# Performance work log

Measured on AMD Instinct MI355X. Metric: run time of the kernel, lower is better.

Reference implementation:

```python
import jax, jax.numpy as jnp
import numpy as np

EPS = 1e-08


def _l2norm(x):
    return x / (jnp.linalg.norm(x, axis=-1, keepdims=True) + EPS)


def _mlp(x, weights):
    # weights: list of (W, b); gelu between layers, none after last
    n = len(weights)
    for i, (W, b) in enumerate(weights):
        x = x @ W + b
        if i < n - 1:
            x = jax.nn.gelu(x)  # approximate gelu, matches jax.nn.gelu default
    return x


def setup_inputs() -> dict:
    key = jax.random.key(0)
    ks = jax.random.split(key, 16)
    N, A, L, K = 65536, 32, 256, 1024
    enc_dims = [A, 512, 1024, L]
    dec_dims = [L, 1024, 512, A]

    def lin(k, din, dout):
        kw, kb = jax.random.split(k)
        W = jax.random.normal(kw, (din, dout), jnp.float32) / np.sqrt(din)
        b = jnp.zeros((dout,), jnp.float32)
        return W, b

    inp = {}
    inp["action"] = jax.random.normal(ks[0], (N, A), jnp.float32)
    inp["dim_weights"] = jax.random.uniform(ks[1], (A,), jnp.float32)
    for i in range(3):
        W, b = lin(ks[2 + i], enc_dims[i], enc_dims[i + 1])
        inp[f"enc_w{i}"], inp[f"enc_b{i}"] = W, b
    for i in range(3):
        W, b = lin(ks[5 + i], dec_dims[i], dec_dims[i + 1])
        inp[f"dec_w{i}"], inp[f"dec_b{i}"] = W, b
    cb = jax.random.normal(ks[8], (K, L), jnp.float32) * 0.1
    inp["codebook"] = _l2norm(cb)
    return inp


def reference(action, dim_weights,
              enc_w0, enc_b0, enc_w1, enc_b1, enc_w2, enc_b2,
              dec_w0, dec_b0, dec_w1, dec_b1, dec_w2, dec_b2,
              codebook):
    enc = [(enc_w0, enc_b0), (enc_w1, enc_b1), (enc_w2, enc_b2)]
    dec = [(dec_w0, dec_b0), (dec_w1, dec_b1), (dec_w2, dec_b2)]

    z_e = _l2norm(_mlp(action, enc))                       # [N, L]
    cb = _l2norm(codebook)                                 # [K, L]
    # squared euclidean distances [N, K]
    dists = (jnp.sum(z_e * z_e, axis=-1, keepdims=True)
             - 2.0 * z_e @ cb.T
             + jnp.sum(cb * cb, axis=-1))
    code_idx = jnp.argmin(dists, axis=-1)                  # [N]
    z_q = cb[code_idx]                                     # [N, L]

    z_q_ste = z_e + jax.lax.stop_gradient(z_q - z_e)
    action_hat = _mlp(z_q_ste, dec)                        # [N, A]

    sq_err = (action - action_hat) ** 2 * dim_weights
    recon_loss = jnp.mean(sq_err)
    codebook_loss = jnp.mean((jax.lax.stop_gradient(z_e) - z_q) ** 2)
    commit_loss = jnp.mean((z_e - jax.lax.stop_gradient(z_q)) ** 2)
    return action_hat, code_idx, recon_loss, codebook_loss, commit_loss
```

## Files before the change

### kernel.cpp

```cpp
#include <hip/hip_runtime.h>
#include <math.h>

#define N_ROWS 65536

typedef short short8 __attribute__((ext_vector_type(8)));
typedef float f32x4 __attribute__((ext_vector_type(4)));

__device__ __forceinline__ float gelu_f(float x) {
  float x3 = x * x * x;
  float t = tanhf(0.7978845608028654f * (x + 0.044715f * x3));
  return 0.5f * x * (1.0f + t);
}

__device__ __forceinline__ unsigned short f2bf(float f) {
  unsigned u = __float_as_uint(f);
  unsigned r = u + 0x7fffu + ((u >> 16) & 1u);
  return (unsigned short)(r >> 16);
}
__device__ __forceinline__ float bf2f(unsigned short h) {
  return __uint_as_float(((unsigned)h) << 16);
}

__device__ __forceinline__ void split3(float v, unsigned short& p0,
                                       unsigned short& p1, unsigned short& p2) {
  p0 = f2bf(v);
  float r = v - bf2f(p0);
  p1 = f2bf(r);
  r -= bf2f(p1);
  p2 = f2bf(r);
}

__device__ __forceinline__ void split3f(float v, unsigned short& p0,
                                        unsigned short& p1, unsigned short& p2) {
  unsigned u = __float_as_uint(v);
  unsigned h0 = (u + 0x8000u) & 0xffff0000u;
  float r = v - __uint_as_float(h0);
  unsigned u1 = __float_as_uint(r);
  unsigned h1 = (u1 + 0x8000u) & 0xffff0000u;
  float r2 = r - __uint_as_float(h1);
  p0 = (unsigned short)(h0 >> 16);
  p1 = (unsigned short)(h1 >> 16);
  p2 = f2bf(r2);
}

__device__ __forceinline__ void split2f(float v, unsigned short& p0,
                                        unsigned short& p1) {
  unsigned u = __float_as_uint(v);
  unsigned h0 = (u + 0x8000u) & 0xffff0000u;
  float r = v - __uint_as_float(h0);
  p0 = (unsigned short)(h0 >> 16);
  p1 = f2bf(r);
}

__device__ __forceinline__ f32x4 mfma16(short8 a, short8 b, f32x4 c) {
  return __builtin_amdgcn_mfma_f32_16x16x32_bf16(a, b, c, 0, 0, 0);
}

template <bool GELU>
__global__ __launch_bounds__(256) void gemm_kernel(
    const float* __restrict__ A, const float* __restrict__ W,
    const float* __restrict__ bias, float* __restrict__ C,
    int din, int dout) {
  __shared__ float As[16][132];
  __shared__ float Ws[16][132];
  int t = threadIdx.x;
  int tx = t & 15, ty = t >> 4;
  int c0 = blockIdx.x * 128;
  int r0 = blockIdx.y * 128;

  float acc[8][8];
#pragma unroll
  for (int i = 0; i < 8; ++i)
#pragma unroll
    for (int j = 0; j < 8; ++j) acc[i][j] = 0.0f;

  int kchunks = din >> 4;
  for (int kc = 0; kc < kchunks; ++kc) {
    int k0 = kc << 4;
    __syncthreads();
#pragma unroll
    for (int it = 0; it < 2; ++it) {
      int id = t + it * 256;
      int r = id >> 2;
      int kq = (id & 3) * 4;
      float4 v = *(const float4*)&A[(long)(r0 + r) * din + (k0 + kq)];
      As[kq + 0][r] = v.x; As[kq + 1][r] = v.y;
      As[kq + 2][r] = v.z; As[kq + 3][r] = v.w;
      int k = id >> 5;
      int cq = (id & 31) * 4;
      float4 w = *(const float4*)&W[(long)(k0 + k) * dout + (c0 + cq)];
      *(float4*)&Ws[k][cq] = w;
    }
    __syncthreads();
#pragma unroll
    for (int k = 0; k < 16; ++k) {
      float av[8], bv[8];
      *(float4*)&av[0] = *(const float4*)&As[k][ty * 4];
      *(float4*)&av[4] = *(const float4*)&As[k][ty * 4 + 64];
      *(float4*)&bv[0] = *(const float4*)&Ws[k][tx * 4];
      *(float4*)&bv[4] = *(const float4*)&Ws[k][tx * 4 + 64];
#pragma unroll
      for (int i = 0; i < 8; ++i)
#pragma unroll
        for (int j = 0; j < 8; ++j)
          acc[i][j] = fmaf(av[i], bv[j], acc[i][j]);
    }
  }

  float bbv[8];
  *(float4*)&bbv[0] = *(const float4*)&bias[c0 + tx * 4];
  *(float4*)&bbv[4] = *(const float4*)&bias[c0 + tx * 4 + 64];
#pragma unroll
  for (int i = 0; i < 8; ++i) {
    long row = r0 + ty * 4 + (i & 3) + ((i >> 2) * 64);
    float o[8];
#pragma unroll
    for (int j = 0; j < 8; ++j) {
      float v = acc[i][j] + bbv[j];
      o[j] = GELU ? gelu_f(v) : v;
    }
    *(float4*)&C[row * dout + c0 + tx * 4] = *(float4*)&o[0];
    *(float4*)&C[row * dout + c0 + tx * 4 + 64] = *(float4*)&o[4];
  }
}

__global__ void frag_pack_kernel(const float* __restrict__ W,
                                 unsigned short* __restrict__ Bf,
                                 int K, int N) {
  int l = threadIdx.x;
  int m = l & 15, q = l >> 4;
  int cb = blockIdx.x, kb = blockIdx.y;
  unsigned short s0[8], s1[8], s2[8];
#pragma unroll
  for (int j = 0; j < 8; ++j) {
    float v = W[(long)(kb * 32 + q * 8 + j) * N + cb * 16 + m];
    split3(v, s0[j], s1[j], s2[j]);
  }
  size_t base = ((size_t)cb * (K / 32) + kb) * 3 * 512;
  *(short8*)&Bf[base + 0 * 512 + l * 8] = *(short8*)s0;
  *(short8*)&Bf[base + 1 * 512 + l * 8] = *(short8*)s1;
  *(short8*)&Bf[base + 2 * 512 + l * 8] = *(short8*)s2;
}

__global__ void frag_pack2_t(const float* __restrict__ cbn,
                             unsigned short* __restrict__ Bf) {
  int l = threadIdx.x;
  int m = l & 15, q = l >> 4;
  int cb = blockIdx.x, kb = blockIdx.y;
  unsigned short s0[8], s1[8];
  const float* src = cbn + (long)(cb * 16 + m) * 256 + kb * 32 + q * 8;
#pragma unroll
  for (int j = 0; j < 8; ++j) split2f(src[j], s0[j], s1[j]);
  size_t base = ((size_t)(cb * 8 + kb) * 2) * 512;
  *(short8*)&Bf[base + l * 8] = *(short8*)s0;
  *(short8*)&Bf[base + 512 + l * 8] = *(short8*)s1;
}

template <bool GELU>
__global__ __launch_bounds__(256) void mfma3_gemm(
    const float* __restrict__ A, const unsigned short* __restrict__ Bf,
    const float* __restrict__ bias, float* __restrict__ C,
    int K, int dout) {
  __shared__ unsigned short A_f[3 * 2 * 4 * 512];
  int t = threadIdx.x;
  int lane = t & 63, wave = t >> 6;
  int q = lane >> 4, m = lane & 15;
  int wrb = wave >> 1;
  int wr = wrb * 64, wc = (wave & 1) * 64;
  long r0 = (long)blockIdx.y * 128;
  int c0 = blockIdx.x * 128;
  int kchunks = K >> 5;

  f32x4 acc[4][4];
#pragma unroll
  for (int i = 0; i < 4; ++i)
#pragma unroll
    for (int j = 0; j < 4; ++j) acc[i][j] = (f32x4){0.f, 0.f, 0.f, 0.f};

  int rs = t >> 1, hs = (t & 1) * 16;
  const float* aptr = A + (r0 + rs) * K + hs;
  int cb0 = (c0 + wc) >> 4;
  int xw = (rs >> 4) & 3, wrbw = rs >> 6, mw = rs & 15;
  int g0 = ((t & 1) * 2 + 0) * 16 + mw;
  int g1 = ((t & 1) * 2 + 1) * 16 + mw;
  int wb0 = (0 * 2 + wrbw) * 4 + xw;
  int wb1 = (1 * 2 + wrbw) * 4 + xw;
  int wb2 = (2 * 2 + wrbw) * 4 + xw;

  for (int kb = 0; kb < kchunks; ++kb) {
    __syncthreads();
    {
      int kt = kb << 5;
      float fv[16];
      *(float4*)&fv[0] = *(const float4*)(aptr + kt + 0);
      *(float4*)&fv[4] = *(const float4*)(aptr + kt + 4);
      *(float4*)&fv[8] = *(const float4*)(aptr + kt + 8);
      *(float4*)&fv[12] = *(const float4*)(aptr + kt + 12);
      unsigned short a0[16], a1[16], a2[16];
#pragma unroll
      for (int i = 0; i < 16; ++i) split3f(fv[i], a0[i], a1[i], a2[i]);
      *(uint4*)&A_f[wb0 * 512 + g0 * 8] = ((uint4*)a0)[0];
      *(uint4*)&A_f[wb0 * 512 + g1 * 8] = ((uint4*)a0)[1];
      *(uint4*)&A_f[wb1 * 512 + g0 * 8] = ((uint4*)a1)[0];
      *(uint4*)&A_f[wb1 * 512 + g1 * 8] = ((uint4*)a1)[1];
      *(uint4*)&A_f[wb2 * 512 + g0 * 8] = ((uint4*)a2)[0];
      *(uint4*)&A_f[wb2 * 512 + g1 * 8] = ((uint4*)a2)[1];
    }
    __syncthreads();
    short8 af[3][4];
#pragma unroll
    for (int p = 0; p < 3; ++p)
#pragma unroll
      for (int x = 0; x < 4; ++x)
        af[p][x] = *(const short8*)&A_f[((p * 2 + wrb) * 4 + x) * 512 + lane * 8];
#pragma unroll
    for (int ct = 0; ct < 4; ++ct) {
      size_t fb = ((size_t)(cb0 + ct) * kchunks + kb) * 3 * 512 + lane * 8;
      short8 b0 = *(const short8*)&Bf[fb];
      short8 b1 = *(const short8*)&Bf[fb + 512];
      short8 b2 = *(const short8*)&Bf[fb + 1024];
#pragma unroll
      for (int rt = 0; rt < 4; ++rt) {
        acc[rt][ct] = mfma16(af[0][rt], b0, acc[rt][ct]);
        acc[rt][ct] = mfma16(af[0][rt], b1, acc[rt][ct]);
        acc[rt][ct] = mfma16(af[1][rt], b0, acc[rt][ct]);
        acc[rt][ct] = mfma16(af[0][rt], b2, acc[rt][ct]);
        acc[rt][ct] = mfma16(af[1][rt], b1, acc[rt][ct]);
        acc[rt][ct] = mfma16(af[2][rt], b0, acc[rt][ct]);
      }
    }
  }

#pragma unroll
  for (int ct = 0; ct < 4; ++ct) {
    long col = c0 + wc + ct * 16 + m;
    float bv = bias[col];
#pragma unroll
    for (int rt = 0; rt < 4; ++rt) {
      long rowb = r0 + wr + rt * 16 + q * 4;
#pragma unroll
      for (int r = 0; r < 4; ++r) {
        float v = acc[rt][ct][r] + bv;
        if (GELU) v = gelu_f(v);
        C[(rowb + r) * dout + col] = v;
      }
    }
  }
}

__global__ __launch_bounds__(256) void dist2_mfma(
    const float* __restrict__ z_e, const unsigned short* __restrict__ cbf,
    int* __restrict__ idxc, int* __restrict__ fixcnt, int* __restrict__ fixlist) {
  __shared__ unsigned short A_f[2 * 8 * 4 * 512];
  __shared__ float Lv1[64][4], Lv2[64][4];
  __shared__ int Lc1[64][4];
  int t = threadIdx.x;
  int lane = t & 63, wave = t >> 6;
  int q = lane >> 4, m = lane & 15;
  long r0 = (long)blockIdx.x * 64;

#pragma unroll
  for (int it = 0; it < 4; ++it) {
    int kb = it * 2 + (t >> 7);
    int rs = (t & 127) >> 1, hs = (t & 1) * 16;
    const float* ap = z_e + (r0 + rs) * 256 + kb * 32 + hs;
    float fv[16];
    *(float4*)&fv[0] = *(const float4*)(ap + 0);
    *(float4*)&fv[4] = *(const float4*)(ap + 4);
    *(float4*)&fv[8] = *(const float4*)(ap + 8);
    *(float4*)&fv[12] = *(const float4*)(ap + 12);
    unsigned short a0[16], a1[16];
#pragma unroll
    for (int i = 0; i < 16; ++i) split2f(fv[i], a0[i], a1[i]);
    int x = rs >> 4, mm = rs & 15;
    int ga = ((t & 1) * 2 + 0) * 16 + mm;
    int gb = ((t & 1) * 2 + 1) * 16 + mm;
    int b0 = ((0 * 8 + kb) * 4 + x) * 512;
    int b1 = ((1 * 8 + kb) * 4 + x) * 512;
    *(uint4*)&A_f[b0 + ga * 8] = ((uint4*)a0)[0];
    *(uint4*)&A_f[b0 + gb * 8] = ((uint4*)a0)[1];
    *(uint4*)&A_f[b1 + ga * 8] = ((uint4*)a1)[0];
    *(uint4*)&A_f[b1 + gb * 8] = ((uint4*)a1)[1];
  }
  __syncthreads();

  float v1[4][4], v2[4][4];
  int c1[4][4];
#pragma unroll
  for (int i = 0; i < 4; ++i)
#pragma unroll
    for (int j = 0; j < 4; ++j) { v1[i][j] = -3.4e38f; v2[i][j] = -3.4e38f; c1[i][j] = 0; }

  for (int ctp = 0; ctp < 4; ++ctp) {
    f32x4 acc[4][4];
#pragma unroll
    for (int i = 0; i < 4; ++i)
#pragma unroll
      for (int j = 0; j < 4; ++j) acc[i][j] = (f32x4){0.f, 0.f, 0.f, 0.f};

    for (int kb = 0; kb < 8; ++kb) {
      short8 af0[4], af1[4];
#pragma unroll
      for (int rt = 0; rt < 4; ++rt) {
        af0[rt] = *(const short8*)&A_f[((0 * 8 + kb) * 4 + rt) * 512 + lane * 8];
        af1[rt] = *(const short8*)&A_f[((1 * 8 + kb) * 4 + rt) * 512 + lane * 8];
      }
      short8 bf0[4], bf1[4];
#pragma unroll
      for (int cs = 0; cs < 4; ++cs) {
        int cb = ctp * 16 + (cs >> 1) * 8 + wave * 2 + (cs & 1);
        size_t fb = ((size_t)(cb * 8 + kb) * 2) * 512 + lane * 8;
        bf0[cs] = *(const short8*)&cbf[fb];
        bf1[cs] = *(const short8*)&cbf[fb + 512];
      }
#pragma unroll
      for (int rt = 0; rt < 4; ++rt)
#pragma unroll
        for (int cs = 0; cs < 4; ++cs) {
          acc[rt][cs] = mfma16(af0[rt], bf0[cs], acc[rt][cs]);
          acc[rt][cs] = mfma16(af0[rt], bf1[cs], acc[rt][cs]);
          acc[rt][cs] = mfma16(af1[rt], bf0[cs], acc[rt][cs]);
        }
    }
#pragma unroll
    for (int rt = 0; rt < 4; ++rt)
#pragma unroll
      for (int cs = 0; cs < 4; ++cs) {
        int colb = ctp * 256 + (cs >> 1) * 128 + wave * 32 + (cs & 1) * 16 + m;
#pragma unroll
        for (int r = 0; r < 4; ++r) {
          float v = acc[rt][cs][r];
          float nv2 = fmaxf(v2[rt][r], fminf(v, v1[rt][r]));
          if (v > v1[rt][r]) { c1[rt][r] = colb; v1[rt][r] = v; }
          v2[rt][r] = nv2;
        }
      }
  }

#pragma unroll
  for (int off = 1; off <= 8; off <<= 1) {
#pragma unroll
    for (int rt = 0; rt < 4; ++rt)
#pragma unroll
      for (int r = 0; r < 4; ++r) {
        float ov1 = __shfl_xor(v1[rt][r], off);
        float ov2 = __shfl_xor(v2[rt][r], off);
        int oc1 = __shfl_xor(c1[rt][r], off);
        float nv2 = fmaxf(fmaxf(v2[rt][r], ov2), fminf(v1[rt][r], ov1));
        if (ov1 > v1[rt][r] || (ov1 == v1[rt][r] && oc1 < c1[rt][r])) {
          v1[rt][r] = ov1; c1[rt][r] = oc1;
        }
        v2[rt][r] = nv2;
      }
  }
  if (m == 0) {
#pragma unroll
    for (int rt = 0; rt < 4; ++rt)
#pragma unroll
      for (int r = 0; r < 4; ++r) {
        int rloc = rt * 16 + q * 4 + r;
        Lv1[rloc][wave] = v1[rt][r];
        Lv2[rloc][wave] = v2[rt][r];
        Lc1[rloc][wave] = c1[rt][r];
      }
  }
  __syncthreads();
  if (t < 64) {
    float a1 = Lv1[t][0], a2 = Lv2[t][0];
    int ac = Lc1[t][0];
#pragma unroll
    for (int w = 1; w < 4; ++w) {
      float b1 = Lv1[t][w], b2 = Lv2[t][w];
      int bc = Lc1[t][w];
      float n2 = fmaxf(fmaxf(a2, b2), fminf(a1, b1));
      if (b1 > a1 || (b1 == a1 && bc < ac)) { a1 = b1; ac = bc; }
      a2 = n2;
    }
    idxc[r0 + t] = ac;
    if (a1 - a2 < 5.0e-4f) {
      int p = atomicAdd(fixcnt, 1);
      fixlist[p] = r0 + t;
    }
  }
}

__global__ __launch_bounds__(256) void fixup_part(
    const float* __restrict__ z_e, const float* __restrict__ cbn,
    const float* __restrict__ ze2, const float* __restrict__ cb2,
    const int* __restrict__ fixlist, const int* __restrict__ fixcnt,
    float* __restrict__ fixbv, int* __restrict__ fixbc) {
  int cnt = *fixcnt;
  int r0 = blockIdx.y * 128;
  if (r0 >= cnt) return;
  int ctile = blockIdx.x;
  int c0 = ctile * 128;
  __shared__ float As[16][132];
  __shared__ float Ws[16][132];
  __shared__ float rv[128][17];
  __shared__ int rc[128][17];
  __shared__ int rows_l[128];
  int t = threadIdx.x, tx = t & 15, ty = t >> 4;

  if (t < 128) rows_l[t] = fixlist[(r0 + t < cnt) ? (r0 + t) : 0];
  __syncthreads();

  float bestv[8];
  int bestc[8];
  float myze2[8];
#pragma unroll
  for (int i = 0; i < 8; ++i) {
    bestv[i] = 3.4e38f;
    bestc[i] = 0;
    int rl = ty * 4 + (i & 3) + ((i >> 2) * 64);
    myze2[i] = ze2[rows_l[rl]];
  }

  float acc[8][8];
#pragma unroll
  for (int i = 0; i < 8; ++i)
#pragma unroll
    for (int j = 0; j < 8; ++j) acc[i][j] = 0.0f;

  for (int kc = 0; kc < 16; ++kc) {
    int k0 = kc << 4;
    __syncthreads();
#pragma unroll
    for (int it = 0; it < 2; ++it) {
      int id = t + it * 256;
      int r = id >> 2;
      int kq = (id & 3) * 4;
      float4 v = *(const float4*)&z_e[(long)rows_l[r] * 256 + k0 + kq];
      As[kq + 0][r] = v.x; As[kq + 1][r] = v.y;
      As[kq + 2][r] = v.z; As[kq + 3][r] = v.w;
      float4 w = *(const float4*)&cbn[(long)(c0 + r) * 256 + k0 + kq];
      Ws[kq + 0][r] = w.x; Ws[kq + 1][r] = w.y;
      Ws[kq + 2][r] = w.z; Ws[kq + 3][r] = w.w;
    }
    __syncthreads();
#pragma unroll
    for (int k = 0; k < 16; ++k) {
      float av[8], bv[8];
      *(float4*)&av[0] = *(const float4*)&As[k][ty * 4];
      *(float4*)&av[4] = *(const float4*)&As[k][ty * 4 + 64];
      *(float4*)&bv[0] = *(const float4*)&Ws[k][tx * 4];
      *(float4*)&bv[4] = *(const float4*)&Ws[k][tx * 4 + 64];
#pragma unroll
      for (int i = 0; i < 8; ++i)
#pragma unroll
        for (int j = 0; j < 8; ++j)
          acc[i][j] = fmaf(av[i], bv[j], acc[i][j]);
    }
  }

  float cb2v[8];
  *(float4*)&cb2v[0] = *(const float4*)&cb2[c0 + tx * 4];
  *(float4*)&cb2v[4] = *(const float4*)&cb2[c0 + tx * 4 + 64];
#pragma unroll
  for (int i = 0; i < 8; ++i)
#pragma unroll
    for (int j = 0; j < 8; ++j) {
      int c = c0 + tx * 4 + (j & 3) + ((j >> 2) * 64);
      float d = (myze2[i] - 2.0f * acc[i][j]) + cb2v[j];
      if (d < bestv[i] || (d == bestv[i] && c < bestc[i])) {
        bestv[i] = d;
        bestc[i] = c;
      }
    }

  __syncthreads();
#pragma unroll
  for (int i = 0; i < 8; ++i) {
    int rl = ty * 4 + (i & 3) + ((i >> 2) * 64);
    rv[rl][tx] = bestv[i];
    rc[rl][tx] = bestc[i];
  }
  __syncthreads();
  if (t < 128 && r0 + t < cnt) {
    float bv = rv[t][0];
    int bc = rc[t][0];
    for (int j = 1; j < 16; ++j) {
      float v = rv[t][j];
      int c = rc[t][j];
      if (v < bv || (v == bv && c < bc)) { bv = v; bc = c; }
    }
    fixbv[(long)(r0 + t) * 8 + ctile] = bv;
    fixbc[(long)(r0 + t) * 8 + ctile] = bc;
  }
}

__global__ __launch_bounds__(256) void fixup_reduce(
    const float* __restrict__ fixbv, const int* __restrict__ fixbc,
    const int* __restrict__ fixlist, const int* __restrict__ fixcnt,
    int* __restrict__ idxc) {
  int cnt = *fixcnt;
  int i = blockIdx.x * 256 + threadIdx.x;
  if (i >= cnt) return;
  float bv = fixbv[(long)i * 8];
  int bc = fixbc[(long)i * 8];
#pragma unroll
  for (int j = 1; j < 8; ++j) {
    float v = fixbv[(long)i * 8 + j];
    int c = fixbc[(long)i * 8 + j];
    if (v < bv || (v == bv && c < bc)) { bv = v; bc = c; }
  }
  idxc[fixlist[i]] = bc;
}

__global__ __launch_bounds__(256) void rownorm_kernel(
    const float* __restrict__ in, float* __restrict__ outv,
    float* __restrict__ outsq) {
  int wid = threadIdx.x >> 6, lane = threadIdx.x & 63;
  long row = (long)blockIdx.x * 4 + wid;
  const float* src = in + row * 256;
  float4 v = *(const float4*)&src[lane * 4];
  float s = v.x * v.x + v.y * v.y + v.z * v.z + v.w * v.w;
#pragma unroll
  for (int off = 32; off >= 1; off >>= 1) s += __shfl_xor(s, off);
  float denom = sqrtf(s) + 1e-8f;
  float4 o;
  o.x = v.x / denom; o.y = v.y / denom; o.z = v.z / denom; o.w = v.w / denom;
  *(float4*)&outv[row * 256 + lane * 4] = o;
  float s2 = o.x * o.x + o.y * o.y + o.z * o.z + o.w * o.w;
#pragma unroll
  for (int off = 32; off >= 1; off >>= 1) s2 += __shfl_xor(s2, off);
  if (lane == 0) outsq[row] = s2;
}

__global__ __launch_bounds__(256) void t2_kernel(
    const float* __restrict__ T1, const float* __restrict__ W,
    const float* __restrict__ bias, float* __restrict__ T2) {
  int id = blockIdx.x * 256 + threadIdx.x;
  int row = id >> 5, col = id & 31;
  const float* a = T1 + (long)row * 512;
  float s = 0.f;
#pragma unroll 8
  for (int k = 0; k < 512; ++k) s = fmaf(a[k], W[k * 32 + col], s);
  T2[id] = s + bias[col];
}

__global__ __launch_bounds__(256) void fused_tail(
    const float* __restrict__ z_e, const float* __restrict__ cbn,
    const int* __restrict__ idxc, const float* __restrict__ T2,
    const float* __restrict__ action, const float* __restrict__ dimw,
    float* __restrict__ partRe, float* __restrict__ partCo,
    float* __restrict__ outIdx, float* __restrict__ ahat, int pb) {
  int t = threadIdx.x, wid = t >> 6, lane = t & 63;
  float cs = 0.f, rsum = 0.f;
#pragma unroll
  for (int r = 0; r < 4; ++r) {
    long row = (long)blockIdx.x * 16 + wid * 4 + r;
    int k = idxc[row];
    float4 a = *(const float4*)&z_e[row * 256 + lane * 4];
    float4 b = *(const float4*)&cbn[(long)k * 256 + lane * 4];
    float dx = a.x - b.x, dy = a.y - b.y, dz = a.z - b.z, dq = a.w - b.w;
    cs += dx * dx + dy * dy + dz * dz + dq * dq;
    if (lane < 8) {
      float4 av = *(const float4*)&action[row * 32 + lane * 4];
      float4 tv = *(const float4*)&T2[(long)k * 32 + lane * 4];
      float4 wv = *(const float4*)&dimw[lane * 4];
      *(float4*)&ahat[row * 32 + lane * 4] = tv;
      float ex = av.x - tv.x, ey = av.y - tv.y;
      float ez = av.z - tv.z, ew = av.w - tv.w;
      rsum += ex * ex * wv.x + ey * ey * wv.y + ez * ez * wv.z + ew * ew * wv.w;
    }
    if (lane == 0) outIdx[row] = (float)k;
  }
#pragma unroll
  for (int off = 32; off >= 1; off >>= 1) {
    cs += __shfl_xor(cs, off);
    rsum += __shfl_xor(rsum, off);
  }
  __shared__ float rc[4], rr[4];
  if (lane == 0) { rc[wid] = cs; rr[wid] = rsum; }
  __syncthreads();
  if (t == 0) {
    partCo[pb + blockIdx.x] = rc[0] + rc[1] + rc[2] + rc[3];
    partRe[pb + blockIdx.x] = rr[0] + rr[1] + rr[2] + rr[3];
  }
}

__global__ void zero_kernel(int* __restrict__ cnts) {
  if (threadIdx.x < 32) cnts[threadIdx.x] = 0;
}

__global__ __launch_bounds__(256) void finalize_kernel(
    const float* __restrict__ partRe, const float* __restrict__ partCo,
    float* __restrict__ out) {
  int t = threadIdx.x;
  float sr = 0.f, sc = 0.f;
  for (int i = t; i < 4096; i += 256) { sr += partRe[i]; sc += partCo[i]; }
#pragma unroll
  for (int off = 32; off >= 1; off >>= 1) {
    sr += __shfl_xor(sr, off);
    sc += __shfl_xor(sc, off);
  }
  __shared__ float rs_[4], cs_[4];
  int wid = t >> 6, lane = t & 63;
  if (lane == 0) { rs_[wid] = sr; cs_[wid] = sc; }
  __syncthreads();
  if (t == 0) {
    float r = rs_[0] + rs_[1] + rs_[2] + rs_[3];
    float c = cs_[0] + cs_[1] + cs_[2] + cs_[3];
    out[0] = r / (65536.0f * 32.0f);
    float cl = c / (65536.0f * 256.0f);
    out[1] = cl;
    out[2] = cl;
  }
}

extern "C" void kernel_launch(void* const* d_in, const int* in_sizes, int n_in,
                              void* d_out, int out_size, void* d_ws,
                              size_t ws_size, hipStream_t stream) {
  const float* action = (const float*)d_in[0];
  const float* dimw = (const float*)d_in[1];
  const float* ew0 = (const float*)d_in[2];
  const float* eb0 = (const float*)d_in[3];
  const float* ew1 = (const float*)d_in[4];
  const float* eb1 = (const float*)d_in[5];
  const float* ew2 = (const float*)d_in[6];
  const float* eb2 = (const float*)d_in[7];
  const float* dw0 = (const float*)d_in[8];
  const float* db0 = (const float*)d_in[9];
  const float* dw1 = (const float*)d_in[10];
  const float* db1 = (const float*)d_in[11];
  const float* dw2 = (const float*)d_in[12];
  const float* db2 = (const float*)d_in[13];
  const float* cb = (const float*)d_in[14];
  float* out = (float*)d_out;
  char* ws = (char*)d_ws;

  const size_t fixed_b = 1048576 + 4096 + 1048576 + 3145728 + 1572864 +
                         4194304 + 2097152 + 131072 + 256 + 32768;
  int R = N_ROWS;
  while (R > 2048) {
    if (fixed_b + (size_t)R * 6220 + 65536 <= ws_size) break;
    R >>= 1;
  }

  size_t off = 0;
  float* cbn = (float*)(ws + off); off += 1048576;
  float* cb2 = (float*)(ws + off); off += 4096;
  unsigned short* cbf = (unsigned short*)(ws + off); off += 1048576;
  unsigned short* ewf1 = (unsigned short*)(ws + off); off += 3145728;
  unsigned short* ewf2 = (unsigned short*)(ws + off); off += 1572864;
  float* T0 = (float*)(ws + off); off += 4194304;
  float* T1d = (float*)(ws + off); off += 2097152;
  float* T2d = (float*)(ws + off); off += 131072;
  int* fixcnts = (int*)(ws + off); off += 256;
  float* partRe = (float*)(ws + off); off += 16384;
  float* partCo = (float*)(ws + off); off += 16384;
  float* ze2 = (float*)(ws + off); off += (size_t)R * 4;
  int* idxc = (int*)(ws + off); off += (size_t)R * 4;
  int* fixlist = (int*)(ws + off); off += (size_t)R * 4;
  float* fixbv = (float*)(ws + off); off += (size_t)R * 32;
  int* fixbc = (int*)(ws + off); off += (size_t)R * 32;
  char* P0 = ws + off; off += (size_t)R * 2048;
  char* P1 = ws + off; off += (size_t)R * 4096;

  float* e0 = (float*)P0;
  float* e1 = (float*)P1;
  float* zbuf = (float*)P0;
  float* z_e = (float*)(P0 + (size_t)R * 1024);

  zero_kernel<<<1, 64, 0, stream>>>(fixcnts);
  rownorm_kernel<<<256, 256, 0, stream>>>(cb, cbn, cb2);
  frag_pack2_t<<<dim3(64, 8), 64, 0, stream>>>(cbn, cbf);
  frag_pack_kernel<<<dim3(64, 16), 64, 0, stream>>>(ew1, ewf1, 512, 1024);
  frag_pack_kernel<<<dim3(16, 32), 64, 0, stream>>>(ew2, ewf2, 1024, 256);

  gemm_kernel<true><<<dim3(8, 8), 256, 0, stream>>>(cbn, dw0, db0, T0, 256, 1024);
  gemm_kernel<true><<<dim3(4, 8), 256, 0, stream>>>(T0, dw1, db1, T1d, 1024, 512);
  t2_kernel<<<128, 256, 0, stream>>>(T1d, dw2, db2, T2d);

  for (int base = 0; base < N_ROWS; base += R) {
    int ci = base / R;
    const float* act_c = action + (size_t)base * 32;
    float* out_c = out + (size_t)base * 32;
    int* fixcnt = &fixcnts[ci];

    gemm_kernel<true><<<dim3(4, R / 128), 256, 0, stream>>>(
        act_c, ew0, eb0, e0, 32, 512);
    mfma3_gemm<true><<<dim3(8, R / 128), 256, 0, stream>>>(
        e0, ewf1, eb1, e1, 512, 1024);
    mfma3_gemm<false><<<dim3(2, R / 128), 256, 0, stream>>>(
        e1, ewf2, eb2, zbuf, 1024, 256);

    rownorm_kernel<<<R / 4, 256, 0, stream>>>(zbuf, z_e, ze2);

    dist2_mfma<<<R / 64, 256, 0, stream>>>(z_e, cbf, idxc, fixcnt, fixlist);
    fixup_part<<<dim3(8, R / 128), 256, 0, stream>>>(
        z_e, cbn, ze2, cb2, fixlist, fixcnt, fixbv, fixbc);
    fixup_reduce<<<R / 256, 256, 0, stream>>>(fixbv, fixbc, fixlist, fixcnt,
                                              idxc);

    fused_tail<<<R / 16, 256, 0, stream>>>(
        z_e, cbn, idxc, T2d, act_c, dimw, partRe, partCo,
        out + 2097152 + base, out_c, base >> 4);
  }

  finalize_kernel<<<1, 256, 0, stream>>>(partRe, partCo, out + 2162688);
}
```

Before: 1.242 ms.

## Fuse final encoder GEMM with L2 row norm and remap block order

Replaces the last encoder GEMM plus separate rownorm kernel with a 512-thread kernel where each block owns 128 full rows of 256 outputs, computing the bias, squared-norm reduction and normalization in registers and writing z_e and ze2 directly. It also adds a block-index swizzle to mfma3_gemm that groups blocks for cache locality, and switches the small decoder-on-codebook GEMMs to a 64x64 tile kernel for more blocks. The aim is to remove the intermediate zbuf round trip and a kernel launch, and to improve occupancy and L2 reuse. The fused kernel launches fewer blocks and uses more threads per block, which could lower parallelism for the 1024-K GEMM.

```diff
diff --git a/kernel.cpp b/kernel.cpp
--- a/kernel.cpp
+++ b/kernel.cpp
@@ -124,6 +124,65 @@
   }
 }
 
+template <bool GELU>
+__global__ __launch_bounds__(256) void gemm64_kernel(
+    const float* __restrict__ A, const float* __restrict__ W,
+    const float* __restrict__ bias, float* __restrict__ C,
+    int din, int dout) {
+  __shared__ float As[16][68];
+  __shared__ float Ws[16][68];
+  int t = threadIdx.x;
+  int tx = t & 15, ty = t >> 4;
+  int c0 = blockIdx.x * 64;
+  int r0 = blockIdx.y * 64;
+
+  float acc[4][4];
+#pragma unroll
+  for (int i = 0; i < 4; ++i)
+#pragma unroll
+    for (int j = 0; j < 4; ++j) acc[i][j] = 0.0f;
+
+  int kchunks = din >> 4;
+  for (int kc = 0; kc < kchunks; ++kc) {
+    int k0 = kc << 4;
+    __syncthreads();
+    {
+      int r = t >> 2, kq = (t & 3) * 4;
+      float4 v = *(const float4*)&A[(long)(r0 + r) * din + (k0 + kq)];
+      As[kq + 0][r] = v.x; As[kq + 1][r] = v.y;
+      As[kq + 2][r] = v.z; As[kq + 3][r] = v.w;
+      int k = t >> 4, cq = (t & 15) * 4;
+      *(float4*)&Ws[k][cq] = *(const float4*)&W[(long)(k0 + k) * dout + (c0 + cq)];
+    }
+    __syncthreads();
+#pragma unroll
+    for (int k = 0; k < 16; ++k) {
+      float av[4], bv[4];
+      *(float4*)&av[0] = *(const float4*)&As[k][ty * 4];
+      *(float4*)&bv[0] = *(const float4*)&Ws[k][tx * 4];
+#pragma unroll
+      for (int i = 0; i < 4; ++i)
+#pragma unroll
+        for (int j = 0; j < 4; ++j)
+          acc[i][j] = fmaf(av[i], bv[j], acc[i][j]);
+    }
+  }
+
+  float4 bb = *(const float4*)&bias[c0 + tx * 4];
+#pragma unroll
+  for (int i = 0; i < 4; ++i) {
+    long row = r0 + ty * 4 + i;
+    float o[4];
+    o[0] = acc[i][0] + bb.x; o[1] = acc[i][1] + bb.y;
+    o[2] = acc[i][2] + bb.z; o[3] = acc[i][3] + bb.w;
+    if (GELU) {
+      o[0] = gelu_f(o[0]); o[1] = gelu_f(o[1]);
+      o[2] = gelu_f(o[2]); o[3] = gelu_f(o[3]);
+    }
+    *(float4*)&C[row * dout + c0 + tx * 4] = *(float4*)&o[0];
+  }
+}
+
 __global__ void frag_pack_kernel(const float* __restrict__ W,
                                  unsigned short* __restrict__ Bf,
                                  int K, int N) {
@@ -167,8 +226,14 @@
   int q = lane >> 4, m = lane & 15;
   int wrb = wave >> 1;
   int wr = wrb * 64, wc = (wave & 1) * 64;
-  long r0 = (long)blockIdx.y * 128;
-  int c0 = blockIdx.x * 128;
+
+  int gx = gridDim.x, tot = gx * gridDim.y;
+  int lin = blockIdx.y * gx + blockIdx.x;
+  if (!(tot & 7)) lin = (lin & 7) * (tot >> 3) + (lin >> 3);
+  int bx = lin % gx, by = lin / gx;
+
+  long r0 = (long)by * 128;
+  int c0 = bx * 128;
   int kchunks = K >> 5;
 
   f32x4 acc[4][4];
@@ -246,6 +311,113 @@
       }
     }
   }
+}
+
+__global__ __launch_bounds__(512) void mfma3_norm(
+    const float* __restrict__ A, const unsigned short* __restrict__ Bf,
+    const float* __restrict__ bias, float* __restrict__ z_e,
+    float* __restrict__ ze2) {
+  __shared__ unsigned short A_f[3 * 2 * 4 * 512];
+  __shared__ float S[128][4];
+  __shared__ float Sinv[128];
+  const int K = 1024, kchunks = 32;
+  int t = threadIdx.x;
+  int lane = t & 63, wave = t >> 6;
+  int q = lane >> 4, m = lane & 15;
+  int wrb = wave >> 2;
+  int wcq = wave & 3;
+  long r0 = (long)blockIdx.x * 128;
+
+  f32x4 acc[4][4];
+#pragma unroll
+  for (int i = 0; i < 4; ++i)
+#pragma unroll
+    for (int j = 0; j < 4; ++j) acc[i][j] = (f32x4){0.f, 0.f, 0.f, 0.f};
+
+  int rs = t >> 2, kq = t & 3;
+  const float* aptr = A + (r0 + rs) * K + kq * 8;
+  int xw = (rs >> 4) & 3, wrbw = rs >> 6, mw = rs & 15;
+  int gw = kq * 16 + mw;
+  int wb0 = (0 * 2 + wrbw) * 4 + xw;
+  int wb1 = (1 * 2 + wrbw) * 4 + xw;
+  int wb2 = (2 * 2 + wrbw) * 4 + xw;
+  int cb0 = wcq * 4;
+
+  for (int kb = 0; kb < kchunks; ++kb) {
+    __syncthreads();
+    {
+      float fv[8];
+      *(float4*)&fv[0] = *(const float4*)(aptr + (kb << 5));
+      *(float4*)&fv[4] = *(const float4*)(aptr + (kb << 5) + 4);
+      unsigned short a0[8], a1[8], a2[8];
+#pragma unroll
+      for (int i = 0; i < 8; ++i) split3f(fv[i], a0[i], a1[i], a2[i]);
+      *(uint4*)&A_f[wb0 * 512 + gw * 8] = *(uint4*)a0;
+      *(uint4*)&A_f[wb1 * 512 + gw * 8] = *(uint4*)a1;
+      *(uint4*)&A_f[wb2 * 512 + gw * 8] = *(uint4*)a2;
+    }
+    __syncthreads();
+    short8 af[3][4];
+#pragma unroll
+    for (int p = 0; p < 3; ++p)
+#pragma unroll
+      for (int x = 0; x < 4; ++x)
+        af[p][x] = *(const short8*)&A_f[((p * 2 + wrb) * 4 + x) * 512 + lane * 8];
+#pragma unroll
+    for (int ct = 0; ct < 4; ++ct) {
+      size_t fb = ((size_t)(cb0 + ct) * kchunks + kb) * 3 * 512 + lane * 8;
+      short8 b0 = *(const short8*)&Bf[fb];
+      short8 b1 = *(const short8*)&Bf[fb + 512];
+      short8 b2 = *(const short8*)&Bf[fb + 1024];
+#pragma unroll
+      for (int rt = 0; rt < 4; ++rt) {
+        acc[rt][ct] = mfma16(af[0][rt], b0, acc[rt][ct]);
+        acc[rt][ct] = mfma16(af[0][rt], b1, acc[rt][ct]);
+        acc[rt][ct] = mfma16(af[1][rt], b0, acc[rt][ct]);
+        acc[rt][ct] = mfma16(af[0][rt], b2, acc[rt][ct]);
+        acc[rt][ct] = mfma16(af[1][rt], b1, acc[rt][ct]);
+        acc[rt][ct] = mfma16(af[2][rt], b0, acc[rt][ct]);
+      }
+    }
+  }
+
+#pragma unroll
+  for (int ct = 0; ct < 4; ++ct) {
+    float bv = bias[wcq * 64 + ct * 16 + m];
+#pragma unroll
+    for (int rt = 0; rt < 4; ++rt)
+#pragma unroll
+      for (int r = 0; r < 4; ++r) acc[rt][ct][r] += bv;
+  }
+
+#pragma unroll
+  for (int rt = 0; rt < 4; ++rt)
+#pragma unroll
+    for (int r = 0; r < 4; ++r) {
+      float s = acc[rt][0][r] * acc[rt][0][r] + acc[rt][1][r] * acc[rt][1][r] +
+                acc[rt][2][r] * acc[rt][2][r] + acc[rt][3][r] * acc[rt][3][r];
+#pragma unroll
+      for (int off = 1; off <= 8; off <<= 1) s += __shfl_xor(s, off);
+      if (m == 0) S[wrb * 64 + rt * 16 + q * 4 + r][wcq] = s;
+    }
+  __syncthreads();
+  if (t < 128) {
+    float s = S[t][0] + S[t][1] + S[t][2] + S[t][3];
+    float den = sqrtf(s) + 1e-8f;
+    Sinv[t] = 1.0f / den;
+    ze2[r0 + t] = s / (den * den);
+  }
+  __syncthreads();
+#pragma unroll
+  for (int rt = 0; rt < 4; ++rt)
+#pragma unroll
+    for (int r = 0; r < 4; ++r) {
+      int rl = wrb * 64 + rt * 16 + q * 4 + r;
+      float inv = Sinv[rl];
+#pragma unroll
+      for (int ct = 0; ct < 4; ++ct)
+        z_e[(r0 + rl) * 256 + wcq * 64 + ct * 16 + m] = acc[rt][ct][r] * inv;
+    }
 }
 
 __global__ __launch_bounds__(256) void dist2_mfma(
@@ -659,7 +831,6 @@
 
   float* e0 = (float*)P0;
   float* e1 = (float*)P1;
-  float* zbuf = (float*)P0;
   float* z_e = (float*)(P0 + (size_t)R * 1024);
 
   zero_kernel<<<1, 64, 0, stream>>>(fixcnts);
@@ -668,8 +839,8 @@
   frag_pack_kernel<<<dim3(64, 16), 64, 0, stream>>>(ew1, ewf1, 512, 1024);
   frag_pack_kernel<<<dim3(16, 32), 64, 0, stream>>>(ew2, ewf2, 1024, 256);
 
-  gemm_kernel<true><<<dim3(8, 8), 256, 0, stream>>>(cbn, dw0, db0, T0, 256, 1024);
-  gemm_kernel<true><<<dim3(4, 8), 256, 0, stream>>>(T0, dw1, db1, T1d, 1024, 512);
+  gemm64_kernel<true><<<dim3(16, 16), 256, 0, stream>>>(cbn, dw0, db0, T0, 256, 1024);
+  gemm64_kernel<true><<<dim3(8, 16), 256, 0, stream>>>(T0, dw1, db1, T1d, 1024, 512);
   t2_kernel<<<128, 256, 0, stream>>>(T1d, dw2, db2, T2d);
 
   for (int base = 0; base < N_ROWS; base += R) {
@@ -682,10 +853,7 @@
         act_c, ew0, eb0, e0, 32, 512);
     mfma3_gemm<true><<<dim3(8, R / 128), 256, 0, stream>>>(
         e0, ewf1, eb1, e1, 512, 1024);
-    mfma3_gemm<false><<<dim3(2, R / 128), 256, 0, stream>>>(
-        e1, ewf2, eb2, zbuf, 1024, 256);
-
-    rownorm_kernel<<<R / 4, 256, 0, stream>>>(zbuf, z_e, ze2);
+    mfma3_norm<<<R / 128, 512, 0, stream>>>(e1, ewf2, eb2, z_e, ze2);
 
     dist2_mfma<<<R / 64, 256, 0, stream>>>(z_e, cbf, idxc, fixcnt, fixlist);
     fixup_part<<<dim3(8, R / 128), 256, 0, stream>>>(
```

Measured after the change: 1.179 ms. 1.05x faster.
